# Optimization experiments

Measured on AMD Instinct MI355X. Metric: run time of the kernel, lower is better.

The kernel has to match this reference:

```python
import jax, jax.numpy as jnp
import numpy as np
import math

B, TU, TM, D, H = 4, 2048, 256, 1024, 16
DH = D // H
PAIRS = D // 2
LAM = 0.7
EPS_PHASE = 1e-8


def balance_norm(x, w, b, bal_w):
    mu = x.mean(-1, keepdims=True)
    var = ((x - mu) ** 2).mean(-1, keepdims=True)
    normed = (x - mu) / jnp.sqrt(var + 1e-6) * w + b
    half = x.shape[-1] // 2
    e1 = (x[..., :half] ** 2).mean(-1, keepdims=True)
    e2 = (x[..., half:] ** 2).mean(-1, keepdims=True)
    imb = (e1 - e2) * bal_w  # (B,T,1)
    corr = jnp.concatenate([
        jnp.broadcast_to(-imb, x[..., :half].shape),
        jnp.broadcast_to(imb, x[..., half:].shape)], axis=-1)
    return normed + corr


def phase_resonance(a, b):
    # a: (B,Tq,D), b: (B,Tk,D). mean_p cos(th_a - th_b) == (cosA@cosB^T + sinA@sinB^T)/pairs
    def to_phase(x):
        x2 = x.reshape(*x.shape[:-1], PAIRS, 2)
        return jnp.arctan2(x2[..., 1] + EPS_PHASE, x2[..., 0] + EPS_PHASE)
    ta, tb = to_phase(a), to_phase(b)
    ca, sa = jnp.cos(ta), jnp.sin(ta)
    cb, sb = jnp.cos(tb), jnp.sin(tb)
    r = (jnp.einsum('bqp,bkp->bqk', ca, cb) + jnp.einsum('bqp,bkp->bqk', sa, sb)) / PAIRS
    return r


def mha(q_in, kv_in, wq, wk, wv, wo, a_gate, e_gate):
    Bq, Tq, _ = q_in.shape
    Tk = kv_in.shape[1]
    q = (q_in @ wq.T).reshape(Bq, Tq, H, DH)
    k = (kv_in @ wk.T).reshape(Bq, Tk, H, DH)
    v = (kv_in @ wv.T).reshape(Bq, Tk, H, DH)
    scores = jnp.einsum('bqhd,bkhd->bhqk', q, k) / math.sqrt(DH)
    attn = jax.nn.softmax(scores, axis=-1)
    ag = a_gate[:, None, :, :]              # (B,1,Tq,1)
    eg = jnp.swapaxes(e_gate[:, None], 2, 3)  # (B,1,1,Tk)
    attn = attn * ag * eg
    attn = attn / (attn.sum(-1, keepdims=True) + 1e-8)
    ctx = jnp.einsum('bhqk,bkhd->bqhd', attn, v).reshape(Bq, Tq, D)
    return ctx @ wo.T


def setup_inputs() -> dict:
    key = jax.random.key(0)
    ks = jax.random.split(key, 16)
    s = 0.02
    return {
        'o_micro': jax.random.normal(ks[0], (B, TU, D), jnp.float32),
        'o_macro': jax.random.normal(ks[1], (B, TM, D), jnp.float32),
        'r_conv_acc': jax.random.normal(ks[2], (B, TM, TU), jnp.float32) * 0.1,
        'r_emer_acc': jax.random.normal(ks[3], (B, TU, TM), jnp.float32) * 0.1,
        'ln_u_w': jnp.ones((D,), jnp.float32),
        'ln_u_b': jnp.zeros((D,), jnp.float32),
        'bw_u': jnp.float32(0.01),
        'ln_m_w': jnp.ones((D,), jnp.float32),
        'ln_m_b': jnp.zeros((D,), jnp.float32),
        'bw_m': jnp.float32(0.01),
        'gu_w': jax.random.normal(ks[4], (1, D), jnp.float32) * s,
        'gu_b': jnp.zeros((1,), jnp.float32),
        'gm_w': jax.random.normal(ks[5], (1, D), jnp.float32) * s,
        'gm_b': jnp.zeros((1,), jnp.float32),
        'conv_q_w': jax.random.normal(ks[6], (D, D), jnp.float32) * s,
        'conv_k_w': jax.random.normal(ks[7], (D, D), jnp.float32) * s,
        'conv_v_w': jax.random.normal(ks[8], (D, D), jnp.float32) * s,
        'conv_out_w': jax.random.normal(ks[9], (D, D), jnp.float32) * s,
        'emer_q_w': jax.random.normal(ks[10], (D, D), jnp.float32) * s,
        'emer_k_w': jax.random.normal(ks[11], (D, D), jnp.float32) * s,
        'emer_v_w': jax.random.normal(ks[12], (D, D), jnp.float32) * s,
        'emer_out_w': jax.random.normal(ks[13], (D, D), jnp.float32) * s,
        'res_alpha': jnp.float32(1.0),
    }


def reference(o_micro, o_macro, r_conv_acc, r_emer_acc,
              ln_u_w, ln_u_b, bw_u, ln_m_w, ln_m_b, bw_m,
              gu_w, gu_b, gm_w, gm_b,
              conv_q_w, conv_k_w, conv_v_w, conv_out_w,
              emer_q_w, emer_k_w, emer_v_w, emer_out_w, res_alpha):
    ou = balance_norm(o_micro, ln_u_w, ln_u_b, bw_u)
    om = balance_norm(o_macro, ln_m_w, ln_m_b, bw_m)
    g_micro = jax.nn.sigmoid(ou @ gu_w.T + gu_b)  # (B,Tu,1)
    g_macro = jax.nn.sigmoid(om @ gm_w.T + gm_b)  # (B,Tm,1)
    r_conv_inst = phase_resonance(om, ou)  # (B,Tm,Tu)
    r_emer_inst = phase_resonance(ou, om)  # (B,Tu,Tm)
    r_conv_new = LAM * r_conv_acc + (1 - LAM) * r_conv_inst
    r_emer_new = LAM * r_emer_acc + (1 - LAM) * r_emer_inst
    r_conv_scalar = jax.nn.sigmoid(res_alpha * r_conv_new.mean(-1, keepdims=True))
    r_emer_scalar = jax.nn.sigmoid(res_alpha * r_emer_new.mean(-1, keepdims=True))
    delta_macro = mha(om, ou, conv_q_w, conv_k_w, conv_v_w, conv_out_w, g_macro, g_micro)
    o_macro_new = o_macro + delta_macro * r_conv_scalar
    delta_micro = mha(ou, om, emer_q_w, emer_k_w, emer_v_w, emer_out_w, g_micro, g_macro)
    o_micro_new = o_micro + delta_micro * r_emer_scalar
    return (o_micro_new, o_macro_new, r_conv_new, r_emer_new)
```

## Files before the change

kernel.cpp:

```cpp
#include <hip/hip_runtime.h>
#include <math.h>

typedef unsigned short u16;
typedef __attribute__((ext_vector_type(8))) short bf16x8;
typedef __attribute__((ext_vector_type(4))) float f32x4;

__device__ __forceinline__ float sigmoidf_(float x) { return 1.0f / (1.0f + __expf(-x)); }
__device__ __forceinline__ u16 f2bf(float v) {
    union { float f; unsigned u; } x; x.f = v;
    unsigned r = x.u + 0x7fffu + ((x.u >> 16) & 1u);
    return (u16)(r >> 16);
}
__device__ __forceinline__ float bf2f(u16 u) {
    union { unsigned u; float f; } x; x.u = ((unsigned)u) << 16; return x.f;
}

#define GLD(src, dst) __builtin_amdgcn_global_load_lds( \
        (const __attribute__((address_space(1))) void*)(src), \
        (__attribute__((address_space(3))) void*)(dst), 16, 0, 0)
#define GLD4(src, dst) __builtin_amdgcn_global_load_lds( \
        (const __attribute__((address_space(1))) void*)(src), \
        (__attribute__((address_space(3))) void*)(dst), 4, 0, 0)

__global__ void __launch_bounds__(256) norm_gate_kernel(
    const float* __restrict__ X,
    const float* __restrict__ w, const float* __restrict__ bvec,
    const float* __restrict__ bw_p,
    const float* __restrict__ gw, const float* __restrict__ gb_p,
    u16* __restrict__ OUT, u16* __restrict__ PN, float* __restrict__ G)
{
    const int row = blockIdx.x * 4 + (threadIdx.x >> 6);
    const int lane = threadIdx.x & 63;
    const float* xr = X + (size_t)row * 1024 + lane * 16;
    float4 xa = ((const float4*)xr)[0];
    float4 xb = ((const float4*)xr)[1];
    float4 xc = ((const float4*)xr)[2];
    float4 xd = ((const float4*)xr)[3];
    float s1 = (xa.x + xa.y + xa.z + xa.w) + (xb.x + xb.y + xb.z + xb.w)
             + (xc.x + xc.y + xc.z + xc.w) + (xd.x + xd.y + xd.z + xd.w);
    float s2 = xa.x * xa.x + xa.y * xa.y + xa.z * xa.z + xa.w * xa.w
             + xb.x * xb.x + xb.y * xb.y + xb.z * xb.z + xb.w * xb.w
             + xc.x * xc.x + xc.y * xc.y + xc.z * xc.z + xc.w * xc.w
             + xd.x * xd.x + xd.y * xd.y + xd.z * xd.z + xd.w * xd.w;
    #pragma unroll
    for (int o = 1; o <= 32; o <<= 1) s1 += __shfl_xor(s1, o);
    float h2 = s2;
    #pragma unroll
    for (int o = 1; o <= 16; o <<= 1) h2 += __shfl_xor(h2, o);
    const float oth = __shfl_xor(h2, 32);
    const float slo = (lane < 32) ? h2 : oth;
    const float shi = (lane < 32) ? oth : h2;
    const float mu = s1 * (1.0f / 1024.0f);
    const float var = (slo + shi) * (1.0f / 1024.0f) - mu * mu;
    const float rstd = rsqrtf(var + 1e-6f);
    const float imb = (slo - shi) * (1.0f / 512.0f) * (*bw_p);
    const float corr = (lane < 32) ? -imb : imb;
    const int i0 = lane * 16;
    const float4* wp = (const float4*)(w + i0);
    const float4* bp = (const float4*)(bvec + i0);
    const float4* gp = (const float4*)(gw + i0);
    float o16[16];
    float gd = 0.0f;
    #pragma unroll
    for (int q = 0; q < 4; ++q) {
        float4 xv = (q == 0) ? xa : (q == 1) ? xb : (q == 2) ? xc : xd;
        float4 wv = wp[q], bv = bp[q], gv = gp[q];
        float t0 = (xv.x - mu) * rstd * wv.x + bv.x + corr;
        float t1 = (xv.y - mu) * rstd * wv.y + bv.y + corr;
        float t2 = (xv.z - mu) * rstd * wv.z + bv.z + corr;
        float t3 = (xv.w - mu) * rstd * wv.w + bv.w + corr;
        gd += t0 * gv.x + t1 * gv.y + t2 * gv.z + t3 * gv.w;
        o16[4 * q + 0] = t0; o16[4 * q + 1] = t1; o16[4 * q + 2] = t2; o16[4 * q + 3] = t3;
    }
    #pragma unroll
    for (int o = 1; o <= 32; o <<= 1) gd += __shfl_xor(gd, o);
    if (lane == 0) G[row] = sigmoidf_(gd + *gb_p);
    u16 ob[16], pn[16];
    #pragma unroll
    for (int j = 0; j < 16; ++j) ob[j] = f2bf(o16[j]);
    #pragma unroll
    for (int j = 0; j < 8; ++j) {
        float px = o16[2 * j] + 1e-8f, py = o16[2 * j + 1] + 1e-8f;
        float rr = rsqrtf(px * px + py * py);
        pn[2 * j] = f2bf(px * rr); pn[2 * j + 1] = f2bf(py * rr);
    }
    *(uint4*)(OUT + (size_t)row * 1024 + i0) = *(uint4*)ob;
    *(uint4*)(OUT + (size_t)row * 1024 + i0 + 8) = *(uint4*)(ob + 8);
    *(uint4*)(PN + (size_t)row * 1024 + i0) = *(uint4*)pn;
    *(uint4*)(PN + (size_t)row * 1024 + i0 + 8) = *(uint4*)(pn + 8);
}

__global__ void __launch_bounds__(256) wconv_kernel(
    const float* w0, const float* w1, const float* w2, const float* w3,
    const float* w4, const float* w5, const float* w6, const float* w7,
    u16* __restrict__ dst)
{
    const float* s;
    switch (blockIdx.y) {
        case 0: s = w0; break; case 1: s = w1; break;
        case 2: s = w2; break; case 3: s = w3; break;
        case 4: s = w4; break; case 5: s = w5; break;
        case 6: s = w6; break; default: s = w7; break;
    }
    long i = (long)blockIdx.x * 1024 + threadIdx.x * 4;
    float4 v = *(const float4*)(s + i);
    u16 o[4] = { f2bf(v.x), f2bf(v.y), f2bf(v.z), f2bf(v.w) };
    *(uint2*)(dst + (long)blockIdx.y * 1048576 + i) = *(uint2*)o;
}

__global__ void __launch_bounds__(256) attn_flash(
    const u16* __restrict__ Q, const u16* __restrict__ K,
    const u16* __restrict__ VT, const float* __restrict__ AG,
    const float* __restrict__ EG, u16* __restrict__ OC,
    int TQ, int TKV, long vbs)
{
    __shared__ __align__(16) u16 shm[21504];
    float* egf = (float*)(shm + 20480);
    const int t = threadIdx.x;
    const int lane = t & 63, w = t >> 6;
    const int l15 = lane & 15, g = lane >> 4;
    const int qt = blockIdx.x, h = blockIdx.y, b = blockIdx.z;
    const long qrow = (long)b * TQ + qt * 64 + w * 16 + l15;
    const u16* Qp = Q + qrow * 1024 + h * 64 + g * 8;
    const bf16x8 qf0 = *(const bf16x8*)(Qp);
    const bf16x8 qf1 = *(const bf16x8*)(Qp + 32);
    const u16* Kp = K + ((long)b * TKV + w * 16 + l15) * 1024 + h * 64 + g * 8;
    const u16* Vp = VT + (long)b * vbs + (long)(h * 64 + w * 16 + l15) * TKV + g * 8;
    const float* egp = EG + (long)b * TKV + lane;

    auto stage = [&](int kvt, int buf) {
        GLD(Kp + (long)kvt * 1024,      shm + buf * 4096 + (w * 2 + 0) * 512);
        GLD(Kp + (long)kvt * 1024 + 32, shm + buf * 4096 + (w * 2 + 1) * 512);
        GLD(Vp + kvt,      shm + 8192 + buf * 4096 + (w * 2 + 0) * 512);
        GLD(Vp + kvt + 32, shm + 8192 + buf * 4096 + (w * 2 + 1) * 512);
        GLD4(egp + kvt, egf + (buf * 4 + w) * 64);
    };

    const int nT = TKV >> 6;
    f32x4 O[4] = {};
    float mrun = -3.0e38f, lrun = 0.0f, serun = 0.0f;
    stage(0, 0);
    for (int i = 0; i < nT; ++i) {
        const int buf = i & 1;
        if (i + 1 < nT) {
            stage((i + 1) << 6, buf ^ 1);
            asm volatile("s_waitcnt vmcnt(5)" ::: "memory");
        } else {
            asm volatile("s_waitcnt vmcnt(0)" ::: "memory");
        }
        __builtin_amdgcn_sched_barrier(0);
        __builtin_amdgcn_s_barrier();
        const u16* kb = shm + buf * 4096;
        const u16* vb = shm + 8192 + buf * 4096;
        f32x4 sa[4] = {};
        #pragma unroll
        for (int kvf = 0; kvf < 4; ++kvf) {
            bf16x8 kf = *(const bf16x8*)(kb + (kvf * 2 + 0) * 512 + lane * 8);
            sa[kvf] = __builtin_amdgcn_mfma_f32_16x16x32_bf16(kf, qf0, sa[kvf], 0, 0, 0);
        }
        #pragma unroll
        for (int kvf = 0; kvf < 4; ++kvf) {
            bf16x8 kf = *(const bf16x8*)(kb + (kvf * 2 + 1) * 512 + lane * 8);
            sa[kvf] = __builtin_amdgcn_mfma_f32_16x16x32_bf16(kf, qf1, sa[kvf], 0, 0, 0);
        }
        float ev[4][4];
        float tmax = -3.0e38f;
        #pragma unroll
        for (int kvf = 0; kvf < 4; ++kvf)
            #pragma unroll
            for (int j = 0; j < 4; ++j) {
                float s = sa[kvf][j] * 0.125f;
                ev[kvf][j] = s;
                tmax = fmaxf(tmax, s);
            }
        tmax = fmaxf(tmax, __shfl_xor(tmax, 16));
        tmax = fmaxf(tmax, __shfl_xor(tmax, 32));
        const float mnew = fmaxf(mrun, tmax);
        const float corr = __expf(mrun - mnew);
        mrun = mnew;
        float suml = 0.0f, sumg = 0.0f;
        unsigned pk[4][2];
        #pragma unroll
        for (int kvf = 0; kvf < 4; ++kvf) {
            float4 eg4 = *(const float4*)(egf + (buf * 4 + w) * 64 + kvf * 16 + 4 * g);
            float e0 = __expf(ev[kvf][0] - mnew);
            float e1 = __expf(ev[kvf][1] - mnew);
            float e2 = __expf(ev[kvf][2] - mnew);
            float e3 = __expf(ev[kvf][3] - mnew);
            suml += (e0 + e1) + (e2 + e3);
            float g0 = e0 * eg4.x, g1 = e1 * eg4.y, g2 = e2 * eg4.z, g3 = e3 * eg4.w;
            sumg += (g0 + g1) + (g2 + g3);
            pk[kvf][0] = (unsigned)f2bf(g0) | ((unsigned)f2bf(g1) << 16);
            pk[kvf][1] = (unsigned)f2bf(g2) | ((unsigned)f2bf(g3) << 16);
        }
        suml += __shfl_xor(suml, 16); suml += __shfl_xor(suml, 32);
        sumg += __shfl_xor(sumg, 16); sumg += __shfl_xor(sumg, 32);
        lrun = lrun * corr + suml;
        serun = serun * corr + sumg;
        #pragma unroll
        for (int fd = 0; fd < 4; ++fd)
            #pragma unroll
            for (int j = 0; j < 4; ++j) O[fd][j] *= corr;
        u16* pw = shm + 16384 + w * 1024;
        #pragma unroll
        for (int kvf = 0; kvf < 4; ++kvf) {
            const int base = (kvf >> 1) * 512
                           + (l15 + 16 * (2 * (kvf & 1) + (g >> 1))) * 8
                           + 4 * (g & 1);
            *(unsigned*)(pw + base) = pk[kvf][0];
            *(unsigned*)(pw + base + 2) = pk[kvf][1];
        }
        #pragma unroll
        for (int ksv = 0; ksv < 2; ++ksv) {
            bf16x8 pf = *(const bf16x8*)(pw + ksv * 512 + lane * 8);
            #pragma unroll
            for (int fd = 0; fd < 4; ++fd) {
                bf16x8 vf = *(const bf16x8*)(vb + (fd * 2 + ksv) * 512 + lane * 8);
                O[fd] = __builtin_amdgcn_mfma_f32_16x16x32_bf16(vf, pf, O[fd], 0, 0, 0);
            }
        }
        if (i + 1 < nT) __builtin_amdgcn_s_barrier();
    }
    const float agv = AG[qrow];
    const float fac = agv / (agv * serun + lrun * 1e-8f);
    __syncthreads();
    u16* tw = shm + w * 1152;
    #pragma unroll
    for (int fd = 0; fd < 4; ++fd) {
        const int d0 = fd * 16 + 4 * g;
        unsigned v01 = (unsigned)f2bf(O[fd][0] * fac) | ((unsigned)f2bf(O[fd][1] * fac) << 16);
        unsigned v23 = (unsigned)f2bf(O[fd][2] * fac) | ((unsigned)f2bf(O[fd][3] * fac) << 16);
        *(unsigned*)(tw + l15 * 72 + d0) = v01;
        *(unsigned*)(tw + l15 * 72 + d0 + 2) = v23;
    }
    const int qr = lane >> 2, part = lane & 3;
    uint4 va = *(const uint4*)(tw + qr * 72 + part * 16);
    uint4 vb2 = *(const uint4*)(tw + qr * 72 + part * 16 + 8);
    u16* op = OC + ((long)b * TQ + qt * 64 + w * 16 + qr) * 1024 + h * 64 + part * 16;
    *(uint4*)(op) = va;
    *(uint4*)(op + 8) = vb2;
}

template<int BN, int EPI>
__global__ void __launch_bounds__(512, (BN == 128) ? 4 : 1) mfma8(
    const u16* __restrict__ A, const u16* __restrict__ B,
    void* __restrict__ C, void* __restrict__ Cx, void* __restrict__ Cy,
    int K, int lda, int ldb,
    const float* __restrict__ base, const float* __restrict__ rs)
{
    constexpr int NR = BN / 64;
    constexpr int RSTRIDE = 8192 + BN * 32;
    __shared__ __align__(16) u16 sh[3 * RSTRIDE];
    const int gx = gridDim.x, gy = gridDim.y;
    const int lin = blockIdx.x + gx * blockIdx.y;
    const int xcd = lin & 7, off = lin >> 3;
    const int lby = gy >> 3;
    const int by = xcd * lby + (off % lby);
    const int bx = off / lby;
    const int t = threadIdx.x;
    const int lane = t & 63, w = t >> 6;
    const int wm = w >> 2, wn = w & 3;
    const long m0 = (long)by * 256;
    const long n0 = (long)bx * BN;
    const int frow = lane & 15, fk = (lane >> 4) * 8;
    const u16* Ag0 = A + (m0 + w * 16 + frow) * lda + fk;
    const u16* Ag1 = Ag0 + 128L * lda;
    const u16* Bg0 = B + (n0 + w * 16 + frow) * ldb + fk;
    const u16* Bg1 = Bg0 + 128L * ldb;

    auto stageA = [&](int i, int r) {
        const int k0 = i << 5;
        u16* d = sh + r * RSTRIDE;
        GLD(Ag0 + k0, d + w * 512);
        GLD(Ag1 + k0, d + (8 + w) * 512);
    };
    auto stageB = [&](int i, int r) {
        const int k0 = i << 5;
        u16* d = sh + r * RSTRIDE;
        GLD(Bg0 + k0, d + 8192 + w * 512);
        if constexpr (BN == 256) GLD(Bg1 + k0, d + 8192 + (8 + w) * 512);
    };

    const int nIter = K >> 5;
    f32x4 acc[8][NR] = {};
    stageA(0, 0); stageB(0, 0);
    stageA(1, 1); stageB(1, 1);
    if constexpr (BN == 256) asm volatile("s_waitcnt vmcnt(4)" ::: "memory");
    else                     asm volatile("s_waitcnt vmcnt(3)" ::: "memory");
    __builtin_amdgcn_sched_barrier(0);
    __builtin_amdgcn_s_barrier();
    int r = 0;
    for (int i = 0; i < nIter; ++i) {
        const bool pre = (i + 2 < nIter);
        int r2 = r + 2; if (r2 >= 3) r2 -= 3;
        const u16* ra = sh + r * RSTRIDE;
        bf16x8 bf[NR], af[4];
        #pragma unroll
        for (int ni = 0; ni < NR; ++ni)
            bf[ni] = *(const bf16x8*)(ra + 8192 + (wn * NR + ni) * 512 + lane * 8);
        #pragma unroll
        for (int mi = 0; mi < 4; ++mi)
            af[mi] = *(const bf16x8*)(ra + (wm * 8 + mi) * 512 + lane * 8);
        if (pre) stageA(i + 2, r2);
        __builtin_amdgcn_s_barrier();
        asm volatile("s_waitcnt lgkmcnt(0)" ::: "memory");
        __builtin_amdgcn_sched_barrier(0);
        __builtin_amdgcn_s_setprio(1);
        #pragma unroll
        for (int mi = 0; mi < 4; ++mi)
            #pragma unroll
            for (int ni = 0; ni < NR; ++ni)
                acc[mi][ni] = __builtin_amdgcn_mfma_f32_16x16x32_bf16(af[mi], bf[ni], acc[mi][ni], 0, 0, 0);
        __builtin_amdgcn_s_setprio(0);
        __builtin_amdgcn_sched_barrier(0);
        __builtin_amdgcn_s_barrier();
        bf16x8 af2[4];
        #pragma unroll
        for (int mi = 0; mi < 4; ++mi)
            af2[mi] = *(const bf16x8*)(ra + (wm * 8 + 4 + mi) * 512 + lane * 8);
        if (pre) stageB(i + 2, r2);
        __builtin_amdgcn_s_barrier();
        asm volatile("s_waitcnt lgkmcnt(0)" ::: "memory");
        __builtin_amdgcn_sched_barrier(0);
        __builtin_amdgcn_s_setprio(1);
        #pragma unroll
        for (int mi = 0; mi < 4; ++mi)
            #pragma unroll
            for (int ni = 0; ni < NR; ++ni)
                acc[4 + mi][ni] = __builtin_amdgcn_mfma_f32_16x16x32_bf16(af2[mi], bf[ni], acc[4 + mi][ni], 0, 0, 0);
        __builtin_amdgcn_s_setprio(0);
        __builtin_amdgcn_sched_barrier(0);
        if (i + 1 < nIter) {
            if (pre) {
                if constexpr (BN == 256) asm volatile("s_waitcnt vmcnt(4)" ::: "memory");
                else                     asm volatile("s_waitcnt vmcnt(3)" ::: "memory");
            } else {
                asm volatile("s_waitcnt vmcnt(0)" ::: "memory");
            }
            __builtin_amdgcn_sched_barrier(0);
            __builtin_amdgcn_s_barrier();
        }
        ++r; if (r >= 3) r = 0;
    }
    const int l15 = lane & 15, l4 = lane >> 4;
    #pragma unroll
    for (int mi = 0; mi < 8; ++mi) {
        #pragma unroll
        for (int ni = 0; ni < NR; ++ni) {
            const long grow0 = m0 + wm * 128 + mi * 16 + l4 * 4;
            const long gcol  = n0 + wn * (BN / 4) + ni * 16 + l15;
            if constexpr (EPI == 3) {
                #pragma unroll
                for (int j = 0; j < 4; ++j) {
                    const long idx = (grow0 + j) * 1024 + gcol;
                    ((float*)C)[idx] = base[idx] + acc[mi][ni][j] * rs[grow0 + j];
                }
            } else {
                const int sec = (int)(n0 >> 10);
                if (sec == 0) {
                    #pragma unroll
                    for (int j = 0; j < 4; ++j)
                        ((u16*)C)[(grow0 + j) * 1024 + gcol] = f2bf(acc[mi][ni][j]);
                } else if (sec == 1) {
                    const long col = gcol - 1024;
                    u16 pkv[4] = { f2bf(acc[mi][ni][0]), f2bf(acc[mi][ni][1]),
                                   f2bf(acc[mi][ni][2]), f2bf(acc[mi][ni][3]) };
                    const long idx = (grow0 >> 11) * 2097152 + col * 2048 + (grow0 & 2047);
                    *(uint2*)&((u16*)Cx)[idx] = *(uint2*)pkv;
                } else {
                    #pragma unroll
                    for (int j = 0; j < 4; ++j)
                        ((u16*)Cy)[(grow0 + j) * 1024 + (gcol - 2048)] = f2bf(acc[mi][ni][j]);
                }
            }
        }
    }
}

template<int BN, int EPI, bool SWZ>
__global__ void __launch_bounds__(256) mfma_nt(
    const u16* __restrict__ A, long zAb, long zAh,
    const u16* __restrict__ B, long zBb, long zBh,
    void* __restrict__ C, long zCb, long zCh,
    void* __restrict__ Cx, void* __restrict__ Cy,
    int K, int lda, int ldb, int ldc, float alpha, int nH, int nsplit,
    const float* __restrict__ base, const float* __restrict__ rs,
    const float* __restrict__ accB, float* __restrict__ OT,
    long zOT, int ldt)
{
    constexpr int NR = BN / 32;
    constexpr int ABUF = 128 * 32;
    constexpr int BBUF = BN * 32;
    __shared__ __align__(16) u16 sh[3 * (ABUF + BBUF)];
    u16* const Ab0 = sh;
    u16* const Bb0 = sh + 3 * ABUF;
    int bx, by, bz;
    if constexpr (SWZ) {
        const int gx = gridDim.x, gy = gridDim.y;
        const int lin = blockIdx.x + gx * blockIdx.y;
        const int xcd = lin & 7, c = lin >> 3;
        const int LBY = gy >> 3;
        const int SPB = 4 * LBY;
        const int sc = c / SPB, rr = c - sc * SPB;
        const int byl = rr >> 2, bxl = rr & 3;
        by = xcd * LBY + byl;
        bx = sc * 4 + bxl;
        bz = 0;
    } else {
        bx = blockIdx.x; by = blockIdx.y; bz = blockIdx.z;
    }
    const int t = threadIdx.x;
    const int lane = t & 63, w = t >> 6;
    const int wr = w >> 1, wc = w & 1;
    const int slab = bz / nsplit, ks = bz - slab * nsplit;
    const int b = slab / nH, h = slab - b * nH;
    const int kchunk = K / nsplit;
    const int kbeg = ks * kchunk, kend = kbeg + kchunk;
    const long m0 = (long)by * 128;
    const long n0 = (long)bx * BN;
    const int frow = lane & 15, fko = (lane >> 4) * 8;
    const u16* gaA = A + zAb * b + zAh * h + (m0 + 32 * w + frow) * lda + fko;
    const u16* gbB;
    if constexpr (BN == 128) gbB = B + zBb * b + zBh * h + (n0 + 32 * w + frow) * ldb + fko;
    else                     gbB = B + zBb * b + zBh * h + (n0 + 16 * w + frow) * ldb + fko;

    auto stage = [&](int kk, int p) {
        u16* ap = Ab0 + p * ABUF;
        u16* bp = Bb0 + p * BBUF;
        GLD(gaA + kk, ap + 2 * w * 512);
        GLD(gaA + 16L * lda + kk, ap + (2 * w + 1) * 512);
        if constexpr (BN == 128) {
            GLD(gbB + kk, bp + 2 * w * 512);
            GLD(gbB + 16L * ldb + kk, bp + (2 * w + 1) * 512);
        } else {
            GLD(gbB + kk, bp + w * 512);
        }
    };

    const int nIter = (kend - kbeg) >> 5;
    f32x4 acc[4][NR] = {};
    stage(kbeg, 0);
    if (nIter > 1) stage(kbeg + 32, 1);
    int cur = 0;
    for (int i = 0; i < nIter; ++i) {
        if (i + 2 < nIter) {
            int p2 = cur + 2; if (p2 >= 3) p2 -= 3;
            stage(kbeg + (i + 2) * 32, p2);
            if constexpr (BN == 128) asm volatile("s_waitcnt vmcnt(8)" ::: "memory");
            else                     asm volatile("s_waitcnt vmcnt(6)" ::: "memory");
        } else if (i + 1 < nIter) {
            if constexpr (BN == 128) asm volatile("s_waitcnt vmcnt(4)" ::: "memory");
            else                     asm volatile("s_waitcnt vmcnt(3)" ::: "memory");
        } else {
            asm volatile("s_waitcnt vmcnt(0)" ::: "memory");
        }
        __builtin_amdgcn_sched_barrier(0);
        __builtin_amdgcn_s_barrier();
        __builtin_amdgcn_sched_barrier(0);
        const u16* ap = Ab0 + cur * ABUF;
        const u16* bp = Bb0 + cur * BBUF;
        bf16x8 af[4], bfr[NR];
        #pragma unroll
        for (int m = 0; m < 4; ++m)
            af[m] = *(const bf16x8*)(ap + (wr * 4 + m) * 512 + lane * 8);
        #pragma unroll
        for (int n = 0; n < NR; ++n)
            bfr[n] = *(const bf16x8*)(bp + (wc * NR + n) * 512 + lane * 8);
        asm volatile("s_waitcnt lgkmcnt(0)" ::: "memory");
        __builtin_amdgcn_sched_barrier(0);
        __builtin_amdgcn_s_barrier();
        #pragma unroll
        for (int m = 0; m < 4; ++m)
            #pragma unroll
            for (int n = 0; n < NR; ++n)
                acc[m][n] = __builtin_amdgcn_mfma_f32_16x16x32_bf16(af[m], bfr[n], acc[m][n], 0, 0, 0);
        cur = (cur == 2) ? 0 : cur + 1;
    }
    const long Coff = zCb * b + zCh * h;
    const int l15 = lane & 15, l4 = lane >> 4;
    #pragma unroll
    for (int m = 0; m < 4; ++m) {
        #pragma unroll
        for (int n = 0; n < NR; ++n) {
            #pragma unroll
            for (int j = 0; j < 4; ++j) {
                const long grow = m0 + wr * 64 + m * 16 + l4 * 4 + j;
                const long gcol = n0 + wc * (BN / 2) + n * 16 + l15;
                const float v = acc[m][n][j] * alpha;
                if constexpr (EPI == 3) {
                    const long idx = grow * ldc + gcol;
                    ((float*)C)[idx] = base[idx] + v * rs[grow];
                } else if constexpr (EPI == 5) {
                    const long idx = Coff + grow * ldc + gcol;
                    ((float*)C)[idx] = 0.7f * base[idx] + 0.3f * v;
                    const long tidx = zOT * b + gcol * (long)ldt + grow;
                    OT[tidx] = 0.7f * accB[tidx] + 0.3f * v;
                } else if constexpr (EPI == 7) {
                    const int sec = (int)(n0 >> 10);
                    if (sec == 0) ((u16*)C)[grow * 1024 + gcol] = f2bf(v);
                    else if (sec == 1) ((u16*)Cx)[grow * 1024 + (gcol - 1024)] = f2bf(v);
                    else {
                        const long col = gcol - 2048;
                        ((u16*)Cy)[(grow >> 8) * 262144 + col * 256 + (grow & 255)] = f2bf(v);
                    }
                }
            }
        }
    }
}

__global__ void __launch_bounds__(256) rowmean_sig_kernel(
    const float* __restrict__ X, int len, float invlen,
    const float* __restrict__ alpha_p, float* __restrict__ OUT)
{
    const int row = blockIdx.x * 4 + (threadIdx.x >> 6);
    const int lane = threadIdx.x & 63;
    const float* xr = X + (long)row * len;
    float s = 0.0f;
    for (int k = lane; k < len; k += 64) s += xr[k];
    for (int o = 32; o > 0; o >>= 1) s += __shfl_xor(s, o);
    if (lane == 0) OUT[row] = sigmoidf_((*alpha_p) * s * invlen);
}

#define MFMA_TAIL nullptr, nullptr, nullptr, nullptr, 0L, 0

extern "C" void kernel_launch(void* const* d_in, const int* in_sizes, int n_in,
                              void* d_out, int out_size, void* d_ws, size_t ws_size,
                              hipStream_t stream)
{
    (void)in_sizes; (void)n_in; (void)out_size; (void)ws_size;
    const float* o_micro    = (const float*)d_in[0];
    const float* o_macro    = (const float*)d_in[1];
    const float* r_conv_acc = (const float*)d_in[2];
    const float* r_emer_acc = (const float*)d_in[3];
    const float* ln_u_w = (const float*)d_in[4];
    const float* ln_u_b = (const float*)d_in[5];
    const float* bw_u   = (const float*)d_in[6];
    const float* ln_m_w = (const float*)d_in[7];
    const float* ln_m_b = (const float*)d_in[8];
    const float* bw_m   = (const float*)d_in[9];
    const float* gu_w   = (const float*)d_in[10];
    const float* gu_b   = (const float*)d_in[11];
    const float* gm_w   = (const float*)d_in[12];
    const float* gm_b   = (const float*)d_in[13];
    const float* wq_c   = (const float*)d_in[14];
    const float* wk_c   = (const float*)d_in[15];
    const float* wv_c   = (const float*)d_in[16];
    const float* wo_c   = (const float*)d_in[17];
    const float* wq_e   = (const float*)d_in[18];
    const float* wk_e   = (const float*)d_in[19];
    const float* wv_e   = (const float*)d_in[20];
    const float* wo_e   = (const float*)d_in[21];
    const float* res_alpha = (const float*)d_in[22];

    float* out = (float*)d_out;
    float* out_micro = out;
    float* out_macro = out + 8388608;
    float* out_rconv = out + 9437184;
    float* out_remer = out + 11534336;

    float* ws = (float*)d_ws;
    u16* OUb = (u16*)ws;
    u16* OMb = (u16*)(ws + 4194304);
    u16* WB  = (u16*)(ws + 4718592);
    u16* Kcb = (u16*)(ws + 8912896);
    u16* VTc = (u16*)(ws + 13107200);
    u16* Qeb = (u16*)(ws + 17301504);
    u16* Qcb = (u16*)(ws + 21495808);
    u16* Keb = (u16*)(ws + 22020096);
    u16* VTe = (u16*)(ws + 22544384);
    u16* PNu = (u16*)(ws + 23068672);
    float* CT = ws + 27262976;
    float* GU = ws + 28311552;
    float* GM = GU + 8192;
    float* RCS = GM + 1024;
    float* RES = RCS + 1024;
    u16* PNm = (u16*)CT;
    u16* CTc = (u16*)CT;
    u16* CTe = Kcb;

    wconv_kernel<<<dim3(1024, 8), 256, 0, stream>>>(wk_c, wv_c, wq_e, wq_c, wk_e, wv_e, wo_c, wo_e, WB);
    norm_gate_kernel<<<2048, 256, 0, stream>>>(o_micro, ln_u_w, ln_u_b, bw_u, gu_w, gu_b, OUb, PNu, GU);
    norm_gate_kernel<<<256, 256, 0, stream>>>(o_macro, ln_m_w, ln_m_b, bw_m, gm_w, gm_b, OMb, PNm, GM);
    mfma_nt<128, 5, false><<<dim3(16, 2, 4), 256, 0, stream>>>(
        PNm, 262144L, 0L, PNu, 2097152L, 0L, out_rconv, 524288L, 0L, nullptr, nullptr,
        1024, 1024, 1024, 2048, 1.0f / 512.0f, 1, 1,
        r_conv_acc, nullptr, r_emer_acc, out_remer, 524288L, 256);
    rowmean_sig_kernel<<<256, 256, 0, stream>>>(out_rconv, 2048, 1.0f / 2048.0f, res_alpha, RCS);
    rowmean_sig_kernel<<<2048, 256, 0, stream>>>(out_remer, 256, 1.0f / 256.0f, res_alpha, RES);
    mfma8<256, 6><<<dim3(12, 32), 512, 0, stream>>>(
        OUb, WB, Kcb, VTc, Qeb, 1024, 1024, 1024, nullptr, nullptr);
    mfma_nt<128, 7, true><<<dim3(24, 8, 1), 256, 0, stream>>>(
        OMb, 0L, 0L, WB + 3 * 1048576, 0L, 0L, Qcb, 0L, 0L, Keb, VTe,
        1024, 1024, 1024, 1024, 1.0f, 1, 1, MFMA_TAIL);
    attn_flash<<<dim3(4, 16, 4), 256, 0, stream>>>(
        Qcb, Kcb, VTc, GM, GU, CTc, 256, 2048, 2097152L);
    mfma_nt<128, 3, false><<<dim3(8, 8, 1), 256, 0, stream>>>(
        CTc, 0L, 0L, WB + 6 * 1048576, 0L, 0L, out_macro, 0L, 0L, nullptr, nullptr,
        1024, 1024, 1024, 1024, 1.0f, 1, 1, o_macro, RCS, nullptr, nullptr, 0L, 0);
    attn_flash<<<dim3(32, 16, 4), 256, 0, stream>>>(
        Qeb, Keb, VTe, GU, GM, CTe, 2048, 256, 262144L);
    mfma8<128, 3><<<dim3(8, 32), 512, 0, stream>>>(
        CTe, WB + 7 * 1048576, out_micro, nullptr, nullptr,
        1024, 1024, 1024, o_micro, RES);
}
```

Baseline: 297.3 us.

## Rewrite 256-row MFMA GEMM as 8-phase quadrant pipeline with K=64 double buffering

Replaces the mfma8 GEMM with mfma256. It stages K tiles of 64 into two dynamic-shared-memory buffers (previously three buffers of K=32) and splits each 128-wide K step into eight quadrant phases. Each phase loads its A/B fragments, issues one chunk of global-to-LDS prefetch, then runs the MFMAs. The goal is to interleave loads with matrix math more finely and cut barrier overhead per unit of compute. The cost is 128KB/96KB of dynamic LDS per block, which forces one block per CU for BN=128 (it was 4 before), and more complex vmcnt accounting.

```diff
diff --git a/kernel.cpp b/kernel.cpp
--- a/kernel.cpp
+++ b/kernel.cpp
@@ -241,16 +241,44 @@
     *(uint4*)(op + 8) = vb2;
 }
 
+#define PHASE(BUF, MQ, NQ, STAGESTMT, VM) do { \
+    bf16x8 af_[4][2], bf_[NRC][2]; \
+    _Pragma("unroll") for (int fr_ = 0; fr_ < 4; ++fr_) \
+      _Pragma("unroll") for (int kk_ = 0; kk_ < 2; ++kk_) \
+        af_[fr_][kk_] = *(const bf16x8*)(sh + (BUF) * BUFSZ + (MQ) * 8192 + (wm * 4 + fr_) * 1024 + kk_ * 512 + lane * 8); \
+    _Pragma("unroll") for (int fc_ = 0; fc_ < NRC; ++fc_) \
+      _Pragma("unroll") for (int kk_ = 0; kk_ < 2; ++kk_) \
+        bf_[fc_][kk_] = *(const bf16x8*)(sh + (BUF) * BUFSZ + 16384 + (NQ) * BHALF + (wn * NRC + fc_) * 1024 + kk_ * 512 + lane * 8); \
+    STAGESTMT \
+    __builtin_amdgcn_s_barrier(); \
+    asm volatile("s_waitcnt lgkmcnt(0)" ::: "memory"); \
+    __builtin_amdgcn_sched_barrier(0); \
+    __builtin_amdgcn_s_setprio(1); \
+    _Pragma("unroll") for (int fr_ = 0; fr_ < 4; ++fr_) \
+      _Pragma("unroll") for (int fc_ = 0; fc_ < NRC; ++fc_) \
+        _Pragma("unroll") for (int kk_ = 0; kk_ < 2; ++kk_) \
+          acc[(MQ) * 4 + fr_][(NQ) * NRC + fc_] = __builtin_amdgcn_mfma_f32_16x16x32_bf16( \
+              af_[fr_][kk_], bf_[fc_][kk_], acc[(MQ) * 4 + fr_][(NQ) * NRC + fc_], 0, 0, 0); \
+    __builtin_amdgcn_s_setprio(0); \
+    __builtin_amdgcn_sched_barrier(0); \
+    if ((VM) == 1) { \
+        if constexpr (BN == 256) asm volatile("s_waitcnt vmcnt(4)" ::: "memory"); \
+        else                     asm volatile("s_waitcnt vmcnt(3)" ::: "memory"); \
+    } else if ((VM) == 2) { asm volatile("s_waitcnt vmcnt(0)" ::: "memory"); } \
+    __builtin_amdgcn_s_barrier(); \
+} while (0)
+
 template<int BN, int EPI>
-__global__ void __launch_bounds__(512, (BN == 128) ? 4 : 1) mfma8(
+__global__ void __launch_bounds__(512, 1) mfma256(
     const u16* __restrict__ A, const u16* __restrict__ B,
     void* __restrict__ C, void* __restrict__ Cx, void* __restrict__ Cy,
     int K, int lda, int ldb,
     const float* __restrict__ base, const float* __restrict__ rs)
 {
-    constexpr int NR = BN / 64;
-    constexpr int RSTRIDE = 8192 + BN * 32;
-    __shared__ __align__(16) u16 sh[3 * RSTRIDE];
+    constexpr int NRC = BN / 128;
+    constexpr int BHALF = BN * 32;
+    constexpr int BUFSZ = 16384 + 2 * BHALF;
+    extern __shared__ u16 sh[];
     const int gx = gridDim.x, gy = gridDim.y;
     const int lin = blockIdx.x + gx * blockIdx.y;
     const int xcd = lin & 7, off = lin >> 3;
@@ -262,116 +290,91 @@
     const int wm = w >> 2, wn = w & 3;
     const long m0 = (long)by * 256;
     const long n0 = (long)bx * BN;
-    const int frow = lane & 15, fk = (lane >> 4) * 8;
-    const u16* Ag0 = A + (m0 + w * 16 + frow) * lda + fk;
-    const u16* Ag1 = Ag0 + 128L * lda;
-    const u16* Bg0 = B + (n0 + w * 16 + frow) * ldb + fk;
-    const u16* Bg1 = Bg0 + 128L * ldb;
-
-    auto stageA = [&](int i, int r) {
-        const int k0 = i << 5;
-        u16* d = sh + r * RSTRIDE;
-        GLD(Ag0 + k0, d + w * 512);
-        GLD(Ag1 + k0, d + (8 + w) * 512);
+    const int l15 = lane & 15, g = lane >> 4;
+
+    auto stageA = [&](int h, int kt, int buf) {
+        const long kb = (long)kt * 64 + g * 8;
+        #pragma unroll
+        for (int r2 = 0; r2 < 2; ++r2) {
+            const int c = w + 8 * r2;
+            const int sub = c >> 1, kc = c & 1;
+            GLD(A + (m0 + h * 128 + sub * 16 + l15) * lda + kb + kc * 32,
+                sh + buf * BUFSZ + h * 8192 + c * 512);
+        }
     };
-    auto stageB = [&](int i, int r) {
-        const int k0 = i << 5;
-        u16* d = sh + r * RSTRIDE;
-        GLD(Bg0 + k0, d + 8192 + w * 512);
-        if constexpr (BN == 256) GLD(Bg1 + k0, d + 8192 + (8 + w) * 512);
+    auto stageB = [&](int h, int kt, int buf) {
+        const long kb = (long)kt * 64 + g * 8;
+        if constexpr (BN == 256) {
+            #pragma unroll
+            for (int r2 = 0; r2 < 2; ++r2) {
+                const int c = w + 8 * r2;
+                const int sub = c >> 1, kc = c & 1;
+                GLD(B + (n0 + h * 128 + sub * 16 + l15) * ldb + kb + kc * 32,
+                    sh + buf * BUFSZ + 16384 + h * BHALF + c * 512);
+            }
+        } else {
+            const int c = w;
+            const int sub = c >> 1, kc = c & 1;
+            GLD(B + (n0 + h * 64 + sub * 16 + l15) * ldb + kb + kc * 32,
+                sh + buf * BUFSZ + 16384 + h * BHALF + c * 512);
+        }
     };
 
-    const int nIter = K >> 5;
-    f32x4 acc[8][NR] = {};
-    stageA(0, 0); stageB(0, 0);
-    stageA(1, 1); stageB(1, 1);
-    if constexpr (BN == 256) asm volatile("s_waitcnt vmcnt(4)" ::: "memory");
-    else                     asm volatile("s_waitcnt vmcnt(3)" ::: "memory");
+    const int nkt = K >> 6, nIter = K >> 7;
+    f32x4 acc[8][2 * NRC] = {};
+
+    stageA(0, 0, 0); stageA(1, 0, 0); stageB(0, 0, 0); stageB(1, 0, 0);
+    stageA(0, 1, 1); stageA(1, 1, 1); stageB(0, 1, 1); stageB(1, 1, 1);
+    if constexpr (BN == 256) asm volatile("s_waitcnt vmcnt(8)" ::: "memory");
+    else                     asm volatile("s_waitcnt vmcnt(6)" ::: "memory");
     __builtin_amdgcn_sched_barrier(0);
     __builtin_amdgcn_s_barrier();
-    int r = 0;
+
     for (int i = 0; i < nIter; ++i) {
-        const bool pre = (i + 2 < nIter);
-        int r2 = r + 2; if (r2 >= 3) r2 -= 3;
-        const u16* ra = sh + r * RSTRIDE;
-        bf16x8 bf[NR], af[4];
-        #pragma unroll
-        for (int ni = 0; ni < NR; ++ni)
-            bf[ni] = *(const bf16x8*)(ra + 8192 + (wn * NR + ni) * 512 + lane * 8);
-        #pragma unroll
-        for (int mi = 0; mi < 4; ++mi)
-            af[mi] = *(const bf16x8*)(ra + (wm * 8 + mi) * 512 + lane * 8);
-        if (pre) stageA(i + 2, r2);
-        __builtin_amdgcn_s_barrier();
-        asm volatile("s_waitcnt lgkmcnt(0)" ::: "memory");
-        __builtin_amdgcn_sched_barrier(0);
-        __builtin_amdgcn_s_setprio(1);
-        #pragma unroll
-        for (int mi = 0; mi < 4; ++mi)
+        const int kt2 = 2 * i + 2, kt3 = 2 * i + 3;
+        const bool s2 = kt2 < nkt, s3 = kt3 < nkt;
+        PHASE(0, 0, 0, { if (i > 0) stageA(0, 2 * i + 1, 1); }, 0);
+        PHASE(0, 1, 0, { if (i > 0) stageB(1, 2 * i + 1, 1); }, 0);
+        PHASE(0, 1, 1, { if (s2) stageB(0, kt2, 0); }, 0);
+        PHASE(0, 0, 1, { if (s2) stageA(1, kt2, 0); }, s2 ? 1 : 2);
+        PHASE(1, 0, 0, { if (s2) { stageA(0, kt2, 0); stageB(1, kt2, 0); } }, 0);
+        PHASE(1, 1, 0, {}, 0);
+        PHASE(1, 1, 1, { if (s3) stageB(0, kt3, 1); }, 0);
+        PHASE(1, 0, 1, { if (s3) stageA(1, kt3, 1); }, 1);
+    }
+
+    #pragma unroll
+    for (int mq = 0; mq < 2; ++mq)
+    #pragma unroll
+    for (int fr = 0; fr < 4; ++fr)
+    #pragma unroll
+    for (int nq = 0; nq < 2; ++nq)
+    #pragma unroll
+    for (int fc = 0; fc < NRC; ++fc) {
+        const long grow0 = m0 + mq * 128 + wm * 64 + fr * 16 + g * 4;
+        const long gcol = n0 + nq * (BN / 2) + wn * (16 * NRC) + fc * 16 + l15;
+        const f32x4 a = acc[mq * 4 + fr][nq * NRC + fc];
+        if constexpr (EPI == 3) {
             #pragma unroll
-            for (int ni = 0; ni < NR; ++ni)
-                acc[mi][ni] = __builtin_amdgcn_mfma_f32_16x16x32_bf16(af[mi], bf[ni], acc[mi][ni], 0, 0, 0);
-        __builtin_amdgcn_s_setprio(0);
-        __builtin_amdgcn_sched_barrier(0);
-        __builtin_amdgcn_s_barrier();
-        bf16x8 af2[4];
-        #pragma unroll
-        for (int mi = 0; mi < 4; ++mi)
-            af2[mi] = *(const bf16x8*)(ra + (wm * 8 + 4 + mi) * 512 + lane * 8);
-        if (pre) stageB(i + 2, r2);
-        __builtin_amdgcn_s_barrier();
-        asm volatile("s_waitcnt lgkmcnt(0)" ::: "memory");
-        __builtin_amdgcn_sched_barrier(0);
-        __builtin_amdgcn_s_setprio(1);
-        #pragma unroll
-        for (int mi = 0; mi < 4; ++mi)
-            #pragma unroll
-            for (int ni = 0; ni < NR; ++ni)
-                acc[4 + mi][ni] = __builtin_amdgcn_mfma_f32_16x16x32_bf16(af2[mi], bf[ni], acc[4 + mi][ni], 0, 0, 0);
-        __builtin_amdgcn_s_setprio(0);
-        __builtin_amdgcn_sched_barrier(0);
-        if (i + 1 < nIter) {
-            if (pre) {
-                if constexpr (BN == 256) asm volatile("s_waitcnt vmcnt(4)" ::: "memory");
-                else                     asm volatile("s_waitcnt vmcnt(3)" ::: "memory");
+            for (int j = 0; j < 4; ++j) {
+                const long idx = (grow0 + j) * 1024 + gcol;
+                ((float*)C)[idx] = base[idx] + a[j] * rs[grow0 + j];
+            }
+        } else {
+            const int sec = (int)(n0 >> 10);
+            if (sec == 0) {
+                #pragma unroll
+                for (int j = 0; j < 4; ++j)
+                    ((u16*)C)[(grow0 + j) * 1024 + gcol] = f2bf(a[j]);
+            } else if (sec == 1) {
+                const long col = gcol - 1024;
+                u16 pk[4] = { f2bf(a[0]), f2bf(a[1]), f2bf(a[2]), f2bf(a[3]) };
+                const long idx = (grow0 >> 11) * 2097152 + col * 2048 + (grow0 & 2047);
+                *(uint2*)&((u16*)Cx)[idx] = *(uint2*)pk;
             } else {
-                asm volatile("s_waitcnt vmcnt(0)" ::: "memory");
-            }
-            __builtin_amdgcn_sched_barrier(0);
-            __builtin_amdgcn_s_barrier();
-        }
-        ++r; if (r >= 3) r = 0;
-    }
-    const int l15 = lane & 15, l4 = lane >> 4;
-    #pragma unroll
-    for (int mi = 0; mi < 8; ++mi) {
-        #pragma unroll
-        for (int ni = 0; ni < NR; ++ni) {
-            const long grow0 = m0 + wm * 128 + mi * 16 + l4 * 4;
-            const long gcol  = n0 + wn * (BN / 4) + ni * 16 + l15;
-            if constexpr (EPI == 3) {
                 #pragma unroll
-                for (int j = 0; j < 4; ++j) {
-                    const long idx = (grow0 + j) * 1024 + gcol;
-                    ((float*)C)[idx] = base[idx] + acc[mi][ni][j] * rs[grow0 + j];
-                }
-            } else {
-                const int sec = (int)(n0 >> 10);
-                if (sec == 0) {
-                    #pragma unroll
-                    for (int j = 0; j < 4; ++j)
-                        ((u16*)C)[(grow0 + j) * 1024 + gcol] = f2bf(acc[mi][ni][j]);
-                } else if (sec == 1) {
-                    const long col = gcol - 1024;
-                    u16 pkv[4] = { f2bf(acc[mi][ni][0]), f2bf(acc[mi][ni][1]),
-                                   f2bf(acc[mi][ni][2]), f2bf(acc[mi][ni][3]) };
-                    const long idx = (grow0 >> 11) * 2097152 + col * 2048 + (grow0 & 2047);
-                    *(uint2*)&((u16*)Cx)[idx] = *(uint2*)pkv;
-                } else {
-                    #pragma unroll
-                    for (int j = 0; j < 4; ++j)
-                        ((u16*)Cy)[(grow0 + j) * 1024 + (gcol - 2048)] = f2bf(acc[mi][ni][j]);
-                }
+                for (int j = 0; j < 4; ++j)
+                    ((u16*)Cy)[(grow0 + j) * 1024 + (gcol - 2048)] = f2bf(a[j]);
             }
         }
     }
@@ -588,7 +591,7 @@
         r_conv_acc, nullptr, r_emer_acc, out_remer, 524288L, 256);
     rowmean_sig_kernel<<<256, 256, 0, stream>>>(out_rconv, 2048, 1.0f / 2048.0f, res_alpha, RCS);
     rowmean_sig_kernel<<<2048, 256, 0, stream>>>(out_remer, 256, 1.0f / 256.0f, res_alpha, RES);
-    mfma8<256, 6><<<dim3(12, 32), 512, 0, stream>>>(
+    mfma256<256, 6><<<dim3(12, 32), 512, 131072, stream>>>(
         OUb, WB, Kcb, VTc, Qeb, 1024, 1024, 1024, nullptr, nullptr);
     mfma_nt<128, 7, true><<<dim3(24, 8, 1), 256, 0, stream>>>(
         OMb, 0L, 0L, WB + 3 * 1048576, 0L, 0L, Qcb, 0L, 0L, Keb, VTe,
@@ -600,7 +603,7 @@
         1024, 1024, 1024, 1024, 1.0f, 1, 1, o_macro, RCS, nullptr, nullptr, 0L, 0);
     attn_flash<<<dim3(32, 16, 4), 256, 0, stream>>>(
         Qeb, Keb, VTe, GU, GM, CTe, 2048, 256, 262144L);
-    mfma8<128, 3><<<dim3(8, 32), 512, 0, stream>>>(
+    mfma256<128, 3><<<dim3(8, 32), 512, 98304, stream>>>(
         CTe, WB + 7 * 1048576, out_micro, nullptr, nullptr,
         1024, 1024, 1024, o_micro, RES);
 }
```

Measured after the change: 303.2 us. No clear change (+2.0%).
